# Optimization experiments

Hardware: AMD Instinct MI355X
Metric: run time of the kernel (lower is better)

The kernel has to match this reference:

```python
import jax, jax.numpy as jnp
import numpy as np


def setup_inputs() -> dict:
    key = jax.random.key(0)
    k1, k2, k3 = jax.random.split(key, 3)
    B, N, D = 8, 4096, 64
    q = jax.random.normal(k1, (B, N, D), dtype=jnp.float32)
    k = jax.random.normal(k2, (B, N, D), dtype=jnp.float32)
    v = jax.random.normal(k3, (B, N, D), dtype=jnp.float32)
    attn_mask = jnp.ones((B, N), dtype=jnp.int32)  # 1 = attend, 0 = padding
    return {"q": q, "k": k, "v": v, "attn_mask": attn_mask}


def reference(q, k, v, attn_mask):
    # q: [B, n_q, d], k/v: [B, n_k, d], attn_mask: [B, n_k]
    d = q.shape[-1]
    n_q, n_k = q.shape[1], k.shape[1]
    scale = jnp.sqrt(jnp.asarray(d, dtype=q.dtype))
    # [B, n_q, n_k] attention logits
    logits = jnp.einsum("bqd,bkd->bqk", q, k) / scale
    # causal (mask_future=True): tril keep-mask over (n_q, n_k)
    causal = jnp.tril(jnp.ones((n_q, n_k), dtype=bool))
    neg_inf = jnp.asarray(-jnp.inf, dtype=logits.dtype)
    logits = jnp.where(causal[None, :, :], logits, neg_inf)
    # padding mask broadcast over query dim: [B, 1, n_k]
    logits = jnp.where(attn_mask[:, None, :] == 0, neg_inf, logits)
    w = jax.nn.softmax(logits, axis=-1)
    return jnp.einsum("bqk,bkd->bqd", w, v)
```

## Files before the change

kernel.cpp:

```cpp
#include <hip/hip_runtime.h>


#define BATCH 8
#define SEQ   4096
#define DIM   64
#define QT    64
#define NKT   (SEQ / 64)

typedef __attribute__((ext_vector_type(8))) short bf16x8;
typedef __attribute__((ext_vector_type(4))) float f32x4;

__device__ inline short f2bf(float f) {
    unsigned u = __builtin_bit_cast(unsigned, f);
    u += 0x7FFFu + ((u >> 16) & 1u);
    return (short)(u >> 16);
}

__device__ inline unsigned pk2bf(float a, float b) {
    unsigned ua = __builtin_bit_cast(unsigned, a) + 0x8000u;
    unsigned ub = __builtin_bit_cast(unsigned, b) + 0x8000u;
    return __builtin_amdgcn_perm(ub, ua, 0x07060302u);
}

__device__ inline float fast_exp2(float x) {
#if __has_builtin(__builtin_amdgcn_exp2f)
    return __builtin_amdgcn_exp2f(x);
#else
    return exp2f(x);
#endif
}

__device__ inline void gl_lds16(const void* g, void* l) {
    __builtin_amdgcn_global_load_lds(
        (const __attribute__((address_space(1))) void*)g,
        (__attribute__((address_space(3))) void*)l, 16, 0, 0);
}

__global__ __launch_bounds__(256)
void prep_kv(const float* __restrict__ kg, const float* __restrict__ vg,
             short* __restrict__ kw, short* __restrict__ vw) {
    const int tile = blockIdx.x;
    const float* kp = kg + (size_t)tile * 64 * DIM;
    const float* vp = vg + (size_t)tile * 64 * DIM;
    short* ko = kw + (size_t)tile * 4096;
    short* vo = vw + (size_t)tile * 4096;
    const int t = threadIdx.x;
#pragma unroll
    for (int i = 0; i < 4; ++i) {
        const int flat = i * 256 + t;
        const int key = flat >> 4, d0 = (flat & 15) * 4;
        const float4 kv = *(const float4*)(kp + (size_t)key * DIM + d0);
        uint2 kpk;
        kpk.x = pk2bf(kv.x, kv.y); kpk.y = pk2bf(kv.z, kv.w);
        *(uint2*)(ko + (((d0 >> 3) << 6) + key) * 8 + (d0 & 7)) = kpk;
        const float4 vv = *(const float4*)(vp + (size_t)key * DIM + d0);
        const int kc = key >> 3, jk = key & 7;
        vo[((kc << 6) + d0 + 0) * 8 + jk] = f2bf(vv.x);
        vo[((kc << 6) + d0 + 1) * 8 + jk] = f2bf(vv.y);
        vo[((kc << 6) + d0 + 2) * 8 + jk] = f2bf(vv.z);
        vo[((kc << 6) + d0 + 3) * 8 + jk] = f2bf(vv.w);
    }
}

__global__ __launch_bounds__(512, 4)
void attn_split(const float* __restrict__ qg, const int* __restrict__ mg,
                float* __restrict__ og, const short* __restrict__ kw,
                const short* __restrict__ vw, float* __restrict__ opart,
                float* __restrict__ lpart) {
    __shared__ __align__(16) char smem[59392];
    short* KbS = (short*)smem;
    short* VbS = (short*)(smem + 16384);
    short* PbS = (short*)(smem + 32768);
    float* Ml  = (float*)(smem + 43008);
    float* OX = (float*)smem;
    float* LB = (float*)(smem + 16384);

    const int t    = threadIdx.x;
    const int w    = t >> 6;
    const int L    = t & 63;
    const int c15  = L & 15;
    const int quad = L >> 4;
    const int qsub = w & 3;
    const int kh   = w >> 2;

    const int id   = blockIdx.x;
    const int b    = id & 7;
    const int r_   = id >> 3;
    const int j    = r_ & 31;
    const int sblk = r_ >> 5;
    const int qL   = 63 - j;

    const float* qp = qg + (size_t)b * SEQ * DIM;
    const int*   mp = mg + (size_t)b * SEQ;
    const short* kwb = kw + (size_t)b * NKT * 4096;
    const short* vwb = vw + (size_t)b * NKT * 4096;
    const float qscale = 0.125f * 1.44269504088896340736f;

    auto stage = [&](int bs, int kt) {
        const short* ks = kwb + (size_t)kt * 4096;
        const short* vs = vwb + (size_t)kt * 4096;
        const int off = w << 9;
        gl_lds16(ks + off + (L << 3), KbS + bs * 4096 + off);
        gl_lds16(vs + off + (L << 3), VbS + bs * 4096 + off);
    };

    short* Pw  = PbS + w * 640;
    float* lqs = lpart + (size_t)(b * 32 + j) * 128;
    float* osl = opart + (size_t)(b * 32 + j) * 4096;

    const int nseg = (sblk == 0) ? 1 : 2;
    for (int seg = 0; seg < nseg; ++seg) {
        int qt, kt0, kt1, mode;
        if (sblk == 0)     { qt = qL; kt0 = 0;  kt1 = 33;     mode = 0; }
        else if (seg == 0) { qt = qL; kt0 = 33; kt1 = qL + 1; mode = 1; }
        else               { qt = j;  kt0 = 0;  kt1 = j + 1;  mode = 2; }

        const int qbase = qt * QT;
        const int qrow  = qbase + qsub * 16 + c15;

        bf16x8 Qf[2];
#pragma unroll
        for (int c = 0; c < 2; ++c) {
            const float* src = qp + (size_t)qrow * DIM + c * 32 + quad * 8;
            float4 x = *(const float4*)(src);
            float4 y = *(const float4*)(src + 4);
            bf16x8 f;
            f[0] = f2bf(x.x * qscale); f[1] = f2bf(x.y * qscale);
            f[2] = f2bf(x.z * qscale); f[3] = f2bf(x.w * qscale);
            f[4] = f2bf(y.x * qscale); f[5] = f2bf(y.y * qscale);
            f[6] = f2bf(y.z * qscale); f[7] = f2bf(y.w * qscale);
            Qf[c] = f;
        }

        for (int i = t; i < (kt1 - kt0) * 64; i += 512) {
            const int key = kt0 * 64 + i;
            Ml[key] = mp[key] ? 0.0f : -1e30f;
        }

        float lsum = 0.0f;
        f32x4 Oacc[4];
#pragma unroll
        for (int nb = 0; nb < 4; ++nb) Oacc[nb] = (f32x4){0.f, 0.f, 0.f, 0.f};

        if (kt1 > kt0) stage(0, kt0);

        for (int kt = kt0; kt < kt1; ++kt) {
            const int cur = (kt - kt0) & 1;
            __syncthreads();
            if (kt + 1 < kt1) stage(cur ^ 1, kt + 1);

            const short* Kt = KbS + cur * 4096;
            const short* Vt = VbS + cur * 4096;

            f32x4 sacc[2];
            sacc[0] = (f32x4){0.f, 0.f, 0.f, 0.f};
            sacc[1] = (f32x4){0.f, 0.f, 0.f, 0.f};
#pragma unroll
            for (int c = 0; c < 2; ++c) {
#pragma unroll
                for (int i = 0; i < 2; ++i) {
                    bf16x8 kf = *(const bf16x8*)&Kt[(((quad + 4 * c) << 6) + (2 * kh + i) * 16 + c15) * 8];
                    sacc[i] = __builtin_amdgcn_mfma_f32_16x16x32_bf16(kf, Qf[c], sacc[i], 0, 0, 0);
                }
            }

            const bool diag = (kt == qt);
#pragma unroll
            for (int i = 0; i < 2; ++i) {
                const int kb = 2 * kh + i;
                const float4 ma = *(const float4*)&Ml[kt * 64 + kb * 16 + quad * 4];
                const float mar[4] = {ma.x, ma.y, ma.z, ma.w};
                float p[4];
#pragma unroll
                for (int r = 0; r < 4; ++r) {
                    float s = sacc[i][r] + mar[r];
                    if (diag) {
                        const int keyg = kt * 64 + kb * 16 + quad * 4 + r;
                        if (keyg > qrow) s = -1e30f;
                    }
                    p[r] = fast_exp2(fminf(s, 80.0f));
                    lsum += p[r];
                }
                uint2 pp;
                pp.x = pk2bf(p[0], p[1]);
                pp.y = pk2bf(p[2], p[3]);
                *(uint2*)&Pw[c15 * 40 + i * 16 + quad * 4] = pp;
            }

            bf16x8 pf = *(const bf16x8*)&Pw[c15 * 40 + quad * 8];
#pragma unroll
            for (int nb = 0; nb < 4; ++nb) {
                bf16x8 vf = *(const bf16x8*)&Vt[(((kh * 4 + quad) << 6) + nb * 16 + c15) * 8];
                Oacc[nb] = __builtin_amdgcn_mfma_f32_16x16x32_bf16(pf, vf, Oacc[nb], 0, 0, 0);
            }
        }

        lsum += __shfl_xor(lsum, 16);
        lsum += __shfl_xor(lsum, 32);

        __syncthreads();
        if (w >= 4) {
            const int g = w & 3;
#pragma unroll
            for (int r = 0; r < 4; ++r) {
                const int q = quad * 4 + r;
#pragma unroll
                for (int nb = 0; nb < 4; ++nb)
                    OX[(g * 16 + q) * 64 + nb * 16 + c15] = Oacc[nb][r];
            }
            if (quad == 0) LB[g * 16 + c15] = lsum;
        }
        __syncthreads();
        if (w < 4) {
            const float ltot = lsum + LB[w * 16 + c15];
            const float inv  = 1.0f / ltot;
            float* dst = (mode == 1) ? osl
                                     : og + ((size_t)b * SEQ + qbase) * DIM;
            if (mode != 2 && L < 16)
                lqs[(mode == 1 ? 64 : 0) + w * 16 + L] = ltot;
#pragma unroll
            for (int r = 0; r < 4; ++r) {
                const float ir = (mode == 2)
                    ? __shfl(inv, (L & 48) + ((L & 48) >> 2) + r) : 1.0f;
                const int rl = w * 16 + quad * 4 + r;
#pragma unroll
                for (int nb = 0; nb < 4; ++nb)
                    dst[(size_t)rl * DIM + nb * 16 + c15] =
                        (Oacc[nb][r] + OX[rl * 64 + nb * 16 + c15]) * ir;
            }
        }
        __syncthreads();
    }
}

__global__ __launch_bounds__(256)
void merge_ql(float* __restrict__ og, const float* __restrict__ opart,
              const float* __restrict__ lpart) {
    const int id = blockIdx.x;
    const int b = id & 7, j = id >> 3;
    const int qL = 63 - j;
    const float* sp = opart + (size_t)(b * 32 + j) * 4096;
    const float* lp = lpart + (size_t)(b * 32 + j) * 128;
    float* op = og + ((size_t)b * SEQ + (size_t)qL * 64) * DIM;
    const int t = threadIdx.x;
#pragma unroll
    for (int i = 0; i < 4; ++i) {
        const int flat = i * 256 + t;
        const int row = flat >> 4;
        const int c4  = (flat & 15) * 4;
        const float inv = 1.0f / (lp[row] + lp[64 + row]);
        const float4 a = *(const float4*)(op + (size_t)row * DIM + c4);
        const float4 p = *(const float4*)(sp + (size_t)row * 64 + c4);
        float4 r;
        r.x = (a.x + p.x) * inv;
        r.y = (a.y + p.y) * inv;
        r.z = (a.z + p.z) * inv;
        r.w = (a.w + p.w) * inv;
        *(float4*)(op + (size_t)row * DIM + c4) = r;
    }
}

template <bool WS>
__global__ __launch_bounds__(512, 4)
void attn_fwd(const float* __restrict__ qg, const float* __restrict__ kg,
              const float* __restrict__ vg, const int* __restrict__ mg,
              float* __restrict__ og, const short* __restrict__ kw,
              const short* __restrict__ vw) {
    __shared__ __align__(16) char smem[59392];
    short* KbS = (short*)smem;
    short* VbS = (short*)(smem + 16384);
    short* PbS = (short*)(smem + 32768);
    float* Ml  = (float*)(smem + 43008);
    float* OX = (float*)smem;
    float* LB = (float*)(smem + 16384);

    const int t    = threadIdx.x;
    const int w    = t >> 6;
    const int L    = t & 63;
    const int c15  = L & 15;
    const int quad = L >> 4;
    const int qsub = w & 3;
    const int kh   = w >> 2;

    const int id = blockIdx.x;
    const int b  = id & 7;
    const int j  = id >> 3;
    const int qb = (j < 32) ? (63 - j) : (j - 32);
    const int qbase  = qb * QT;
    const int ntiles = qb + 1;

    const float* qp = qg + (size_t)b * SEQ * DIM;
    const float* kp = kg + (size_t)b * SEQ * DIM;
    const float* vp = vg + (size_t)b * SEQ * DIM;
    const int*   mp = mg + (size_t)b * SEQ;
    const short* kwb = WS ? kw + (size_t)b * NKT * 4096 : nullptr;
    const short* vwb = WS ? vw + (size_t)b * NKT * 4096 : nullptr;

    const int qrow = qbase + qsub * 16 + c15;
    const float qscale = 0.125f * 1.44269504088896340736f;

    bf16x8 Qf[2];
#pragma unroll
    for (int c = 0; c < 2; ++c) {
        const float* src = qp + (size_t)qrow * DIM + c * 32 + quad * 8;
        float4 x = *(const float4*)(src);
        float4 y = *(const float4*)(src + 4);
        bf16x8 f;
        f[0] = f2bf(x.x * qscale); f[1] = f2bf(x.y * qscale);
        f[2] = f2bf(x.z * qscale); f[3] = f2bf(x.w * qscale);
        f[4] = f2bf(y.x * qscale); f[5] = f2bf(y.y * qscale);
        f[6] = f2bf(y.z * qscale); f[7] = f2bf(y.w * qscale);
        Qf[c] = f;
    }

    auto stage = [&](int bs, int kt) {
        const short* ks = kwb + (size_t)kt * 4096;
        const short* vs = vwb + (size_t)kt * 4096;
        const int off = w << 9;
        gl_lds16(ks + off + (L << 3), KbS + bs * 4096 + off);
        gl_lds16(vs + off + (L << 3), VbS + bs * 4096 + off);
    };

    for (int i = t; i < ntiles * 64; i += 512)
        Ml[i] = mp[i] ? 0.0f : -1e30f;

    float lsum = 0.0f;
    f32x4 Oacc[4];
#pragma unroll
    for (int nb = 0; nb < 4; ++nb) Oacc[nb] = (f32x4){0.f, 0.f, 0.f, 0.f};

    if constexpr (WS) stage(0, 0);

    short* Pw = PbS + w * 640;

    for (int kt = 0; kt < ntiles; ++kt) {
        const int cur = WS ? (kt & 1) : 0;

        if constexpr (!WS) {
            __syncthreads();
#pragma unroll
            for (int it = 0; it < 2; ++it) {
                const int flat = it * 512 + t;
                const int key = flat >> 4, d0 = (flat & 15) * 4;
                const float4 kv = *(const float4*)(kp + (size_t)(kt * 64 + key) * DIM + d0);
                uint2 kk;
                kk.x = pk2bf(kv.x, kv.y); kk.y = pk2bf(kv.z, kv.w);
                *(uint2*)&KbS[(((d0 >> 3) << 6) + key) * 8 + (d0 & 7)] = kk;
                const float4 vv = *(const float4*)(vp + (size_t)(kt * 64 + key) * DIM + d0);
                const int kc = key >> 3, jk = key & 7;
                VbS[((kc << 6) + d0 + 0) * 8 + jk] = f2bf(vv.x);
                VbS[((kc << 6) + d0 + 1) * 8 + jk] = f2bf(vv.y);
                VbS[((kc << 6) + d0 + 2) * 8 + jk] = f2bf(vv.z);
                VbS[((kc << 6) + d0 + 3) * 8 + jk] = f2bf(vv.w);
            }
            __syncthreads();
        } else {
            __syncthreads();
            if (kt + 1 < ntiles) stage(cur ^ 1, kt + 1);
        }

        const short* Kt = KbS + cur * 4096;
        const short* Vt = VbS + cur * 4096;

        f32x4 sacc[2];
        sacc[0] = (f32x4){0.f, 0.f, 0.f, 0.f};
        sacc[1] = (f32x4){0.f, 0.f, 0.f, 0.f};
#pragma unroll
        for (int c = 0; c < 2; ++c) {
#pragma unroll
            for (int i = 0; i < 2; ++i) {
                bf16x8 kf = *(const bf16x8*)&Kt[(((quad + 4 * c) << 6) + (2 * kh + i) * 16 + c15) * 8];
                sacc[i] = __builtin_amdgcn_mfma_f32_16x16x32_bf16(kf, Qf[c], sacc[i], 0, 0, 0);
            }
        }

        const bool diag = (kt == ntiles - 1);
#pragma unroll
        for (int i = 0; i < 2; ++i) {
            const int kb = 2 * kh + i;
            const float4 ma = *(const float4*)&Ml[kt * 64 + kb * 16 + quad * 4];
            const float mar[4] = {ma.x, ma.y, ma.z, ma.w};
            float p[4];
#pragma unroll
            for (int r = 0; r < 4; ++r) {
                float s = sacc[i][r] + mar[r];
                if (diag) {
                    const int keyg = kt * 64 + kb * 16 + quad * 4 + r;
                    if (keyg > qrow) s = -1e30f;
                }
                p[r] = fast_exp2(fminf(s, 80.0f));
                lsum += p[r];
            }
            uint2 pp;
            pp.x = pk2bf(p[0], p[1]);
            pp.y = pk2bf(p[2], p[3]);
            *(uint2*)&Pw[c15 * 40 + i * 16 + quad * 4] = pp;
        }

        bf16x8 pf = *(const bf16x8*)&Pw[c15 * 40 + quad * 8];
#pragma unroll
        for (int nb = 0; nb < 4; ++nb) {
            bf16x8 vf = *(const bf16x8*)&Vt[(((kh * 4 + quad) << 6) + nb * 16 + c15) * 8];
            Oacc[nb] = __builtin_amdgcn_mfma_f32_16x16x32_bf16(pf, vf, Oacc[nb], 0, 0, 0);
        }
    }

    lsum += __shfl_xor(lsum, 16);
    lsum += __shfl_xor(lsum, 32);

    __syncthreads();
    if (w >= 4) {
        const int g = w & 3;
#pragma unroll
        for (int r = 0; r < 4; ++r) {
            const int q = quad * 4 + r;
#pragma unroll
            for (int nb = 0; nb < 4; ++nb)
                OX[(g * 16 + q) * 64 + nb * 16 + c15] = Oacc[nb][r];
        }
        if (quad == 0) LB[g * 16 + c15] = lsum;
    }
    __syncthreads();
    if (w < 4) {
        const float inv = 1.0f / (lsum + LB[w * 16 + c15]);
        float* op = og + (size_t)b * SEQ * DIM;
#pragma unroll
        for (int r = 0; r < 4; ++r) {
            const float ir = __shfl(inv, (L & 48) + ((L & 48) >> 2) + r);
            const int row = qbase + w * 16 + quad * 4 + r;
#pragma unroll
            for (int nb = 0; nb < 4; ++nb)
                op[(size_t)row * DIM + nb * 16 + c15] =
                    (Oacc[nb][r] + OX[(w * 16 + quad * 4 + r) * 64 + nb * 16 + c15]) * ir;
        }
    }
}

extern "C" void kernel_launch(void* const* d_in, const int* in_sizes, int n_in,
                              void* d_out, int out_size, void* d_ws, size_t ws_size,
                              hipStream_t stream) {
    (void)in_sizes; (void)n_in; (void)out_size;
    const float* q = (const float*)d_in[0];
    const float* k = (const float*)d_in[1];
    const float* v = (const float*)d_in[2];
    const int*   m = (const int*)d_in[3];
    float* o = (float*)d_out;

    const size_t needKV    = (size_t)BATCH * NKT * 4096 * sizeof(short) * 2;
    const size_t opartB    = (size_t)BATCH * 32 * 4096 * sizeof(float);
    const size_t lpartB    = (size_t)BATCH * 32 * 128 * sizeof(float);
    const size_t needSplit = needKV + opartB + lpartB;

    if (ws_size >= needSplit) {
        short* kw = (short*)d_ws;
        short* vw = kw + (size_t)BATCH * NKT * 4096;
        float* opart = (float*)((char*)d_ws + needKV);
        float* lpart = opart + (size_t)BATCH * 32 * 4096;
        prep_kv<<<dim3(BATCH * NKT), 256, 0, stream>>>(k, v, kw, vw);
        attn_split<<<dim3(512), 512, 0, stream>>>(q, m, o, kw, vw, opart, lpart);
        merge_ql<<<dim3(256), 256, 0, stream>>>(o, opart, lpart);
    } else if (ws_size >= needKV) {
        short* kw = (short*)d_ws;
        short* vw = kw + (size_t)BATCH * NKT * 4096;
        prep_kv<<<dim3(BATCH * NKT), 256, 0, stream>>>(k, v, kw, vw);
        attn_fwd<true><<<dim3(512), 512, 0, stream>>>(q, k, v, m, o, kw, vw);
    } else {
        attn_fwd<false><<<dim3(512), 512, 0, stream>>>(q, k, v, m, o, nullptr, nullptr);
    }
}
```

Before: 124.7 us.

## Split causal attention work into three chunks per query pair with precomputed mask

Repartitions the paired causal query tiles across 768 blocks instead of 512. Each block processes about 22 key tiles, so load is balanced more finely over the CUs. The additive padding mask is now precomputed once in prep_kv into a float workspace and read from global memory, which removes the per-segment LDS mask fill. That shrinks shared memory so launch bounds can allow six blocks per CU. The merge kernel now combines up to three partial outputs, which adds partial-result traffic and more complex segment bookkeeping.

Result: no change. 124.0 us (-0.6%).

```diff
diff --git a/kernel.cpp b/kernel.cpp
--- a/kernel.cpp
+++ b/kernel.cpp
@@ -38,13 +38,18 @@
 
 __global__ __launch_bounds__(256)
 void prep_kv(const float* __restrict__ kg, const float* __restrict__ vg,
-             short* __restrict__ kw, short* __restrict__ vw) {
+             const int* __restrict__ mg, short* __restrict__ kw,
+             short* __restrict__ vw, float* __restrict__ mf) {
     const int tile = blockIdx.x;
     const float* kp = kg + (size_t)tile * 64 * DIM;
     const float* vp = vg + (size_t)tile * 64 * DIM;
     short* ko = kw + (size_t)tile * 4096;
     short* vo = vw + (size_t)tile * 4096;
     const int t = threadIdx.x;
+    if (mf && t < 64) {
+        const int* mp = mg + (size_t)tile * 64;
+        mf[(size_t)tile * 64 + t] = mp[t] ? 0.0f : -1e30f;
+    }
 #pragma unroll
     for (int i = 0; i < 4; ++i) {
         const int flat = i * 256 + t;
@@ -62,16 +67,15 @@
     }
 }
 
-__global__ __launch_bounds__(512, 4)
-void attn_split(const float* __restrict__ qg, const int* __restrict__ mg,
-                float* __restrict__ og, const short* __restrict__ kw,
-                const short* __restrict__ vw, float* __restrict__ opart,
-                float* __restrict__ lpart) {
-    __shared__ __align__(16) char smem[59392];
+__global__ __launch_bounds__(512, 6)
+void attn_split3(const float* __restrict__ qg, float* __restrict__ og,
+                 const short* __restrict__ kw, const short* __restrict__ vw,
+                 const float* __restrict__ mf, float* __restrict__ opart,
+                 float* __restrict__ lpart) {
+    __shared__ __align__(16) char smem[43008];
     short* KbS = (short*)smem;
     short* VbS = (short*)(smem + 16384);
     short* PbS = (short*)(smem + 32768);
-    float* Ml  = (float*)(smem + 43008);
     float* OX = (float*)smem;
     float* LB = (float*)(smem + 16384);
 
@@ -83,17 +87,20 @@
     const int qsub = w & 3;
     const int kh   = w >> 2;
 
-    const int id   = blockIdx.x;
-    const int b    = id & 7;
-    const int r_   = id >> 3;
-    const int j    = r_ & 31;
-    const int sblk = r_ >> 5;
-    const int qL   = 63 - j;
-
-    const float* qp = qg + (size_t)b * SEQ * DIM;
-    const int*   mp = mg + (size_t)b * SEQ;
+    const int id  = blockIdx.x;
+    const int b   = id & 7;
+    const int r_  = id >> 3;
+    const int j   = r_ & 31;
+    const int ch  = r_ >> 5;
+    const int nL  = 64 - j;
+    const int qLt = 63 - j;
+
+    const float* qp  = qg + (size_t)b * SEQ * DIM;
+    const float* mb  = mf + (size_t)b * SEQ;
     const short* kwb = kw + (size_t)b * NKT * 4096;
     const short* vwb = vw + (size_t)b * NKT * 4096;
+    float* osl = opart + (size_t)(b * 32 + j) * 8192;
+    float* lsl = lpart + (size_t)(b * 32 + j) * 256;
     const float qscale = 0.125f * 1.44269504088896340736f;
 
     auto stage = [&](int bs, int kt) {
@@ -104,16 +111,41 @@
         gl_lds16(vs + off + (L << 3), VbS + bs * 4096 + off);
     };
 
-    short* Pw  = PbS + w * 640;
-    float* lqs = lpart + (size_t)(b * 32 + j) * 128;
-    float* osl = opart + (size_t)(b * 32 + j) * 4096;
-
-    const int nseg = (sblk == 0) ? 1 : 2;
+    short* Pw = PbS + w * 640;
+
+    int sqt[2], sk0[2], sk1[2], smode[2], sos[2], sls[2], nseg;
+    sos[0] = sos[1] = 0; sls[0] = sls[1] = 0;
+    if (ch == 0) {
+        nseg = 1;
+        sqt[0] = qLt; sk0[0] = 0;  sk1[0] = 22; smode[0] = 0; sls[0] = 0;
+    } else if (ch == 1) {
+        if (nL >= 44) {
+            nseg = 1;
+            sqt[0] = qLt; sk0[0] = 22; sk1[0] = 44; smode[0] = 1; sos[0] = 0; sls[0] = 1;
+        } else {
+            nseg = 2;
+            sqt[0] = qLt; sk0[0] = 22; sk1[0] = nL;      smode[0] = 1; sos[0] = 0; sls[0] = 1;
+            sqt[1] = j;   sk0[1] = 0;  sk1[1] = 44 - nL; smode[1] = 0; sls[1] = 3;
+        }
+    } else {
+        if (nL > 44) {
+            nseg = 2;
+            sqt[0] = qLt; sk0[0] = 44; sk1[0] = nL;    smode[0] = 1; sos[0] = 1; sls[0] = 2;
+            sqt[1] = j;   sk0[1] = 0;  sk1[1] = j + 1; smode[1] = 2;
+        } else if (nL == 44) {
+            nseg = 1;
+            sqt[0] = j; sk0[0] = 0; sk1[0] = j + 1; smode[0] = 2;
+        } else {
+            nseg = 1;
+            sqt[0] = j; sk0[0] = 44 - nL; sk1[0] = j + 1; smode[0] = 1; sos[0] = 1; sls[0] = 2;
+        }
+    }
+
     for (int seg = 0; seg < nseg; ++seg) {
-        int qt, kt0, kt1, mode;
-        if (sblk == 0)     { qt = qL; kt0 = 0;  kt1 = 33;     mode = 0; }
-        else if (seg == 0) { qt = qL; kt0 = 33; kt1 = qL + 1; mode = 1; }
-        else               { qt = j;  kt0 = 0;  kt1 = j + 1;  mode = 2; }
+        const int qt   = sqt[seg];
+        const int kt0  = sk0[seg];
+        const int kt1  = sk1[seg];
+        const int mode = smode[seg];
 
         const int qbase = qt * QT;
         const int qrow  = qbase + qsub * 16 + c15;
@@ -132,17 +164,12 @@
             Qf[c] = f;
         }
 
-        for (int i = t; i < (kt1 - kt0) * 64; i += 512) {
-            const int key = kt0 * 64 + i;
-            Ml[key] = mp[key] ? 0.0f : -1e30f;
-        }
-
         float lsum = 0.0f;
         f32x4 Oacc[4];
 #pragma unroll
         for (int nb = 0; nb < 4; ++nb) Oacc[nb] = (f32x4){0.f, 0.f, 0.f, 0.f};
 
-        if (kt1 > kt0) stage(0, kt0);
+        stage(0, kt0);
 
         for (int kt = kt0; kt < kt1; ++kt) {
             const int cur = (kt - kt0) & 1;
@@ -168,7 +195,7 @@
 #pragma unroll
             for (int i = 0; i < 2; ++i) {
                 const int kb = 2 * kh + i;
-                const float4 ma = *(const float4*)&Ml[kt * 64 + kb * 16 + quad * 4];
+                const float4 ma = *(const float4*)&mb[kt * 64 + kb * 16 + quad * 4];
                 const float mar[4] = {ma.x, ma.y, ma.z, ma.w};
                 float p[4];
 #pragma unroll
@@ -214,10 +241,10 @@
         if (w < 4) {
             const float ltot = lsum + LB[w * 16 + c15];
             const float inv  = 1.0f / ltot;
-            float* dst = (mode == 1) ? osl
+            float* dst = (mode == 1) ? osl + (size_t)sos[seg] * 4096
                                      : og + ((size_t)b * SEQ + qbase) * DIM;
             if (mode != 2 && L < 16)
-                lqs[(mode == 1 ? 64 : 0) + w * 16 + L] = ltot;
+                lsl[sls[seg] * 64 + w * 16 + L] = ltot;
 #pragma unroll
             for (int r = 0; r < 4; ++r) {
                 const float ir = (mode == 2)
@@ -234,29 +261,60 @@
 }
 
 __global__ __launch_bounds__(256)
-void merge_ql(float* __restrict__ og, const float* __restrict__ opart,
-              const float* __restrict__ lpart) {
+void merge3(float* __restrict__ og, const float* __restrict__ opart,
+            const float* __restrict__ lpart) {
     const int id = blockIdx.x;
     const int b = id & 7, j = id >> 3;
-    const int qL = 63 - j;
-    const float* sp = opart + (size_t)(b * 32 + j) * 4096;
-    const float* lp = lpart + (size_t)(b * 32 + j) * 128;
-    float* op = og + ((size_t)b * SEQ + (size_t)qL * 64) * DIM;
+    const int nL = 64 - j, qLt = 63 - j;
+    const float* os = opart + (size_t)(b * 32 + j) * 8192;
+    const float* ls = lpart + (size_t)(b * 32 + j) * 256;
     const int t = threadIdx.x;
+    const bool hasC = (nL > 44);
+
+    float* opL = og + ((size_t)b * SEQ + (size_t)qLt * 64) * DIM;
 #pragma unroll
     for (int i = 0; i < 4; ++i) {
         const int flat = i * 256 + t;
         const int row = flat >> 4;
         const int c4  = (flat & 15) * 4;
-        const float inv = 1.0f / (lp[row] + lp[64 + row]);
-        const float4 a = *(const float4*)(op + (size_t)row * DIM + c4);
-        const float4 p = *(const float4*)(sp + (size_t)row * 64 + c4);
+        float l = ls[row] + ls[64 + row];
+        if (hasC) l += ls[128 + row];
+        const float inv = 1.0f / l;
+        const float4 a  = *(const float4*)(opL + (size_t)row * DIM + c4);
+        const float4 p0 = *(const float4*)(os + (size_t)row * 64 + c4);
         float4 r;
-        r.x = (a.x + p.x) * inv;
-        r.y = (a.y + p.y) * inv;
-        r.z = (a.z + p.z) * inv;
-        r.w = (a.w + p.w) * inv;
-        *(float4*)(op + (size_t)row * DIM + c4) = r;
+        if (hasC) {
+            const float4 p1 = *(const float4*)(os + 4096 + (size_t)row * 64 + c4);
+            r.x = (a.x + p0.x + p1.x) * inv;
+            r.y = (a.y + p0.y + p1.y) * inv;
+            r.z = (a.z + p0.z + p1.z) * inv;
+            r.w = (a.w + p0.w + p1.w) * inv;
+        } else {
+            r.x = (a.x + p0.x) * inv;
+            r.y = (a.y + p0.y) * inv;
+            r.z = (a.z + p0.z) * inv;
+            r.w = (a.w + p0.w) * inv;
+        }
+        *(float4*)(opL + (size_t)row * DIM + c4) = r;
+    }
+
+    if (nL < 44) {
+        float* opS = og + ((size_t)b * SEQ + (size_t)j * 64) * DIM;
+#pragma unroll
+        for (int i = 0; i < 4; ++i) {
+            const int flat = i * 256 + t;
+            const int row = flat >> 4;
+            const int c4  = (flat & 15) * 4;
+            const float inv = 1.0f / (ls[192 + row] + ls[128 + row]);
+            const float4 a  = *(const float4*)(opS + (size_t)row * DIM + c4);
+            const float4 p1 = *(const float4*)(os + 4096 + (size_t)row * 64 + c4);
+            float4 r;
+            r.x = (a.x + p1.x) * inv;
+            r.y = (a.y + p1.y) * inv;
+            r.z = (a.z + p1.z) * inv;
+            r.w = (a.w + p1.w) * inv;
+            *(float4*)(opS + (size_t)row * DIM + c4) = r;
+        }
     }
 }
 
@@ -446,23 +504,25 @@
     const int*   m = (const int*)d_in[3];
     float* o = (float*)d_out;
 
-    const size_t needKV    = (size_t)BATCH * NKT * 4096 * sizeof(short) * 2;
-    const size_t opartB    = (size_t)BATCH * 32 * 4096 * sizeof(float);
-    const size_t lpartB    = (size_t)BATCH * 32 * 128 * sizeof(float);
-    const size_t needSplit = needKV + opartB + lpartB;
-
-    if (ws_size >= needSplit) {
+    const size_t kvB    = (size_t)BATCH * NKT * 4096 * sizeof(short);
+    const size_t maddB  = (size_t)BATCH * SEQ * sizeof(float);
+    const size_t opartB = (size_t)BATCH * 32 * 8192 * sizeof(float);
+    const size_t lpartB = (size_t)BATCH * 32 * 256 * sizeof(float);
+    const size_t need3  = 2 * kvB + maddB + opartB + lpartB;
+
+    if (ws_size >= need3) {
         short* kw = (short*)d_ws;
         short* vw = kw + (size_t)BATCH * NKT * 4096;
-        float* opart = (float*)((char*)d_ws + needKV);
-        float* lpart = opart + (size_t)BATCH * 32 * 4096;
-        prep_kv<<<dim3(BATCH * NKT), 256, 0, stream>>>(k, v, kw, vw);
-        attn_split<<<dim3(512), 512, 0, stream>>>(q, m, o, kw, vw, opart, lpart);
-        merge_ql<<<dim3(256), 256, 0, stream>>>(o, opart, lpart);
-    } else if (ws_size >= needKV) {
+        float* mf = (float*)((char*)d_ws + 2 * kvB);
+        float* opart = (float*)((char*)d_ws + 2 * kvB + maddB);
+        float* lpart = opart + (size_t)BATCH * 32 * 8192;
+        prep_kv<<<dim3(BATCH * NKT), 256, 0, stream>>>(k, v, m, kw, vw, mf);
+        attn_split3<<<dim3(768), 512, 0, stream>>>(q, o, kw, vw, mf, opart, lpart);
+        merge3<<<dim3(256), 256, 0, stream>>>(o, opart, lpart);
+    } else if (ws_size >= 2 * kvB) {
         short* kw = (short*)d_ws;
         short* vw = kw + (size_t)BATCH * NKT * 4096;
-        prep_kv<<<dim3(BATCH * NKT), 256, 0, stream>>>(k, v, kw, vw);
+        prep_kv<<<dim3(BATCH * NKT), 256, 0, stream>>>(k, v, m, kw, vw, nullptr);
         attn_fwd<true><<<dim3(512), 512, 0, stream>>>(q, k, v, m, o, kw, vw);
     } else {
         attn_fwd<false><<<dim3(512), 512, 0, stream>>>(q, k, v, m, o, nullptr, nullptr);
```
